# Kernel tuning notes

Hardware: AMD Instinct MI355X
Metric: run time of the kernel (lower is better)

Reference implementation:

```python
import jax, jax.numpy as jnp
import numpy as np

N = 100000      # nodes
E = 3200000     # edges
G = 512         # graphs in batch
H = 64          # hidden_channels
EPS = 1e-5      # BatchNorm eps


def _bn(x, g, b, rm, rv):
    # eval-mode BatchNorm1d using running stats
    return (x - rm) * (g * jax.lax.rsqrt(rv + EPS)) + b


def _gcn(x, W, b, src, dst):
    # PyG GCNConv: add self-loops, sym-normalized scatter-add aggregation
    h = x @ W                                  # [N, H]
    deg = jnp.zeros((N,), x.dtype).at[dst].add(1.0) + 1.0  # +1 self-loop
    dinv = jax.lax.rsqrt(deg)                  # deg^{-1/2}
    coef = (dinv[src] * dinv[dst])[:, None]    # per-edge norm
    agg = jax.ops.segment_sum(h[src] * coef, dst, num_segments=N)
    agg = agg + h * (dinv * dinv)[:, None]     # self-loop message
    return agg + b


def setup_inputs() -> dict:
    key = jax.random.key(0)
    ks = jax.random.split(key, 16)
    d = {}
    d['x'] = jax.random.normal(ks[0], (N, 1), jnp.float32)
    d['src'] = jax.random.randint(ks[1], (E,), 0, N, jnp.int32)
    d['dst'] = jax.random.randint(ks[2], (E,), 0, N, jnp.int32)
    d['batch'] = jnp.sort(jax.random.randint(ks[3], (N,), 0, G, jnp.int32))
    def lin(k, fi, fo):
        s = 1.0 / np.sqrt(fi)
        kw, kb = jax.random.split(k)
        return (jax.random.uniform(kw, (fi, fo), jnp.float32, -s, s),
                jax.random.uniform(kb, (fo,), jnp.float32, -s, s))
    d['w1'], d['b1'] = lin(ks[4], 1, H)
    d['w2'], d['b2'] = lin(ks[5], H, H)
    d['w3'], d['b3'] = lin(ks[6], H, H)
    d['wl1'], d['bl1'] = lin(ks[7], 2 * H, H)
    d['wl2'], d['bl2'] = lin(ks[8], H, 2)
    for i, nm in enumerate(['bn1', 'bn2', 'bn3', 'bnl']):
        kk = jax.random.split(ks[9 + i], 2)
        d[nm + '_g'] = jnp.ones((H,), jnp.float32)
        d[nm + '_b'] = jnp.zeros((H,), jnp.float32)
        d[nm + '_rm'] = 0.1 * jax.random.normal(kk[0], (H,), jnp.float32)
        d[nm + '_rv'] = jnp.abs(1.0 + 0.1 * jax.random.normal(kk[1], (H,), jnp.float32))
    return d


def reference(x, src, dst, batch, w1, b1, w2, b2, w3, b3, wl1, bl1, wl2, bl2,
              bn1_g, bn1_b, bn1_rm, bn1_rv, bn2_g, bn2_b, bn2_rm, bn2_rv,
              bn3_g, bn3_b, bn3_rm, bn3_rv, bnl_g, bnl_b, bnl_rm, bnl_rv):
    # eval mode: dropout is identity, BN uses running stats
    h = jax.nn.relu(_bn(_gcn(x, w1, b1, src, dst), bn1_g, bn1_b, bn1_rm, bn1_rv))
    h = jax.nn.relu(_bn(_gcn(h, w2, b2, src, dst), bn2_g, bn2_b, bn2_rm, bn2_rv))
    h = jax.nn.relu(_bn(_gcn(h, w3, b3, src, dst), bn3_g, bn3_b, bn3_rm, bn3_rv))
    # global mean / max pooling over graphs
    cnt = jax.ops.segment_sum(jnp.ones((N,), h.dtype), batch, num_segments=G)
    x_mean = jax.ops.segment_sum(h, batch, num_segments=G) / jnp.maximum(cnt, 1.0)[:, None]
    x_max = jax.ops.segment_max(h, batch, num_segments=G)
    z = jnp.concatenate([x_mean, x_max], axis=1)          # [G, 2H]
    z = jax.nn.relu(_bn(z @ wl1 + bl1, bnl_g, bnl_b, bnl_rm, bnl_rv))
    return z @ wl2 + bl2                                   # [G, 2]
```

## Files before the change

kernel.cpp:

```cpp
#include <hip/hip_runtime.h>
#include <hip/hip_bf16.h>
#include <cstdio>

#define N_NODES 100000
#define E_EDGES 3200000
#define N_GRAPH 512
#define HDIM 64
#define BN_EPS 1e-5f
#define NBUCKET ((N_NODES + 255) / 256)
#define NCHUNK 256
#define CHUNK ((E_EDGES + NCHUNK - 1) / NCHUNK)
#define SORT_CAP 12288
#define NPW 8
#define WT_STRIDE 68

typedef _Float16 f16;
typedef _Float16 half8 __attribute__((ext_vector_type(8)));


__global__ __launch_bounds__(256) void hist_k(const int* __restrict__ dst,
                                              int* __restrict__ histT) {
    __shared__ int h[NBUCKET];
    int c = blockIdx.x, t = threadIdx.x;
    for (int i = t; i < NBUCKET; i += 256) h[i] = 0;
    __syncthreads();
    int e0 = c * CHUNK;
    int e1 = min(e0 + CHUNK, E_EDGES);
    for (int e = e0 + t; e < e1; e += 256)
        atomicAdd(&h[__builtin_nontemporal_load(dst + e) >> 8], 1);
    __syncthreads();
    for (int i = t; i < NBUCKET; i += 256) histT[i * NCHUNK + c] = h[i];
}

__global__ void scanA_k(const int* __restrict__ histT, int* __restrict__ bucket_base,
                        const float* __restrict__ w1, const float* __restrict__ b1,
                        const float* __restrict__ bg1, const float* __restrict__ bb1,
                        const float* __restrict__ brm1, const float* __restrict__ brv1,
                        float2* __restrict__ m1c1) {
    __shared__ int sh[512];
    int t = threadIdx.x;
    if (t < HDIM) {
        float sc1 = bg1[t] * rsqrtf(brv1[t] + BN_EPS);
        m1c1[t] = make_float2(sc1 * w1[t], (b1[t] - brm1[t]) * sc1 + bb1[t]);
    }
    int sum = 0;
    if (t < NBUCKET) {
        const int* row = histT + t * NCHUNK;
        for (int c = 0; c < NCHUNK; c++) sum += row[c];
    }
    sh[t] = sum;
    __syncthreads();
    for (int off = 1; off < 512; off <<= 1) {
        int add = (t >= off) ? sh[t - off] : 0;
        __syncthreads();
        sh[t] += add;
        __syncthreads();
    }
    if (t < NBUCKET) bucket_base[t] = sh[t] - sum;
    if (t == 0) bucket_base[NBUCKET] = E_EDGES;
}

__global__ __launch_bounds__(NCHUNK) void scanB_k(const int* __restrict__ histT,
                                                  const int* __restrict__ bucket_base,
                                                  int* __restrict__ scannedT) {
    __shared__ int sh[NCHUNK];
    int b = blockIdx.x, t = threadIdx.x;
    int v = histT[b * NCHUNK + t];
    sh[t] = v;
    __syncthreads();
    for (int off = 1; off < NCHUNK; off <<= 1) {
        int add = (t >= off) ? sh[t - off] : 0;
        __syncthreads();
        sh[t] += add;
        __syncthreads();
    }
    scannedT[b * NCHUNK + t] = bucket_base[b] + sh[t] - v;
}

__global__ __launch_bounds__(256) void scatter_k(const int* __restrict__ src,
                                                 const int* __restrict__ dst,
                                                 const int* __restrict__ scannedT,
                                                 int* __restrict__ staging) {
    __shared__ int lcnt[NBUCKET];
    int c = blockIdx.x, t = threadIdx.x;
    for (int i = t; i < NBUCKET; i += 256) lcnt[i] = scannedT[i * NCHUNK + c];
    __syncthreads();
    int e0 = c * CHUNK;
    int e1 = min(e0 + CHUNK, E_EDGES);
    for (int e = e0 + t; e < e1; e += 256) {
        int v = __builtin_nontemporal_load(dst + e);
        int u = __builtin_nontemporal_load(src + e);
        int pos = atomicAdd(&lcnt[v >> 8], 1);
        staging[pos] = u | ((v & 255) << 17);
    }
}


__global__ __launch_bounds__(256) void nodeptr_k(const int* __restrict__ staging,
                                                 const int* __restrict__ bucket_base,
                                                 const float* __restrict__ x,
                                                 int* __restrict__ ptr_raw,
                                                 float* __restrict__ dinv,
                                                 float* __restrict__ xtil,
                                                 int* __restrict__ pbt) {
    __shared__ int hn[256];
    __shared__ int sc[256];
    int t = threadIdx.x, b = blockIdx.x;
    int v0 = b << 8;
    int p0 = bucket_base[b], p1 = bucket_base[b + 1];
    hn[t] = 0;
    __syncthreads();
    int cnt = p1 - p0;
    for (int i = t; i < cnt; i += 256)
        atomicAdd(&hn[staging[p0 + i] >> 17], 1);
    __syncthreads();
    int my = hn[t];
    sc[t] = my;
    __syncthreads();
    for (int off = 1; off < 256; off <<= 1) {
        int add = (t >= off) ? sc[t - off] : 0;
        __syncthreads();
        sc[t] += add;
        __syncthreads();
    }
    int v = v0 + t;
    if (v < N_NODES) {
        ptr_raw[v] = p0 + sc[t] - my;
        float dv = rsqrtf((float)(my + 1));
        dinv[v] = dv;
        xtil[v] = dv * x[v];
    }
    if (b == NBUCKET - 1 && t == 0) ptr_raw[N_NODES] = E_EDGES;
    int pd = (my + 3) & ~3;
    __syncthreads();
    sc[t] = pd;
    __syncthreads();
    for (int off = 1; off < 256; off <<= 1) {
        int add = (t >= off) ? sc[t - off] : 0;
        __syncthreads();
        sc[t] += add;
        __syncthreads();
    }
    if (t == 255) pbt[b] = sc[255];
}

__global__ void scanC_k(const int* __restrict__ pbt, int* __restrict__ pbbase,
                        int* __restrict__ ptr_pad) {
    __shared__ int sh[512];
    int t = threadIdx.x;
    int v = (t < NBUCKET) ? pbt[t] : 0;
    sh[t] = v;
    __syncthreads();
    for (int off = 1; off < 512; off <<= 1) {
        int add = (t >= off) ? sh[t - off] : 0;
        __syncthreads();
        sh[t] += add;
        __syncthreads();
    }
    if (t < NBUCKET) pbbase[t] = sh[t] - v;
    if (t == NBUCKET - 1) {
        pbbase[NBUCKET] = sh[t];
        ptr_pad[N_NODES] = sh[t];
        ptr_pad[N_NODES + 1] = sh[t];
    }
}


__global__ __launch_bounds__(256) void csr_l1_k(const int* __restrict__ staging,
                                                const int* __restrict__ ptr_raw,
                                                const int* __restrict__ bucket_base,
                                                const int* __restrict__ pbbase,
                                                const float* __restrict__ dinv,
                                                const float* __restrict__ xtil,
                                                const float* __restrict__ x,
                                                int* __restrict__ csr,
                                                int* __restrict__ ptr_pad,
                                                float2* __restrict__ pairs) {
    __shared__ int lbase[257];
    __shared__ int plp[257];
    __shared__ int ss[256];
    __shared__ int lcnt[256];
    __shared__ int lds_u[SORT_CAP];
    int t = threadIdx.x, b = blockIdx.x;
    int v0 = b << 8;
    int p0 = bucket_base[b];
    int pb0 = pbbase[b];
    for (int i = t; i < 257; i += 256) {
        int vv = v0 + i;
        lbase[i] = ptr_raw[(vv < N_NODES) ? vv : N_NODES] - p0;
    }
    lcnt[t] = 0;
    __syncthreads();
    int deg = lbase[t + 1] - lbase[t];
    int pd = (deg + 3) & ~3;
    ss[t] = pd;
    __syncthreads();
    for (int off = 1; off < 256; off <<= 1) {
        int add = (t >= off) ? ss[t - off] : 0;
        __syncthreads();
        ss[t] += add;
        __syncthreads();
    }
    plp[t] = ss[t] - pd;
    if (t == 255) plp[256] = ss[255];
    __syncthreads();
    int pcnt = plp[256];
    int cnt = lbase[256];
    int4 sent = {N_NODES, N_NODES, N_NODES, N_NODES};
    int lim4 = min(pcnt, SORT_CAP) >> 2;
    for (int i = t; i < lim4; i += 256) ((int4*)lds_u)[i] = sent;
    __syncthreads();
    for (int i = t; i < cnt; i += 256) {
        int packed = staging[p0 + i];
        int u = packed & 0x1FFFF;
        int vl = packed >> 17;
        int r = atomicAdd(&lcnt[vl], 1);
        int pos = plp[vl] + r;
        if (pos < SORT_CAP) lds_u[pos] = u;
        else csr[pb0 + pos] = u;
    }
    __syncthreads();
    for (int i = t; i < lim4; i += 256)
        ((int4*)(csr + pb0))[i] = ((int4*)lds_u)[i];
    __syncthreads();
    int v = v0 + t;
    if (v < N_NODES) {
        int j0 = plp[t];
        for (int j = j0 + deg; j < j0 + pd; j++)
            if (j >= SORT_CAP) csr[pb0 + j] = N_NODES;
        ptr_pad[v] = pb0 + j0;
        float s = 0.f;
        for (int j = j0; j < j0 + deg; j++) {
            int u = (j < SORT_CAP) ? lds_u[j] : csr[pb0 + j];
            s += xtil[u];
        }
        float dv = dinv[v];
        pairs[v] = make_float2(dv * s + dv * dv * x[v], dv);
    }
    if (b == 0 && t == 0) pairs[N_NODES] = make_float2(0.f, 0.f);
}


__global__ __launch_bounds__(256, 4) void agg_l2_k(
    const float2* __restrict__ pairs, const float2* __restrict__ m1c1,
    f16* __restrict__ xout,
    const int* __restrict__ ptr_pad, const int* __restrict__ csr,
    const float* __restrict__ W2, const float* __restrict__ bias2,
    const float* __restrict__ bg2, const float* __restrict__ bb2,
    const float* __restrict__ brm2, const float* __restrict__ brv2) {
    __shared__ float wsh_t[HDIM * WT_STRIDE];
    __shared__ float sM[HDIM], sC[HDIM];
    __shared__ float a_lds[4][HDIM];
    __shared__ float occ_pad[4096];
    int tid = threadIdx.x;
    occ_pad[tid] = 0.f;
    for (int i = tid; i < HDIM * HDIM; i += 256)
        wsh_t[(i & 63) * WT_STRIDE + (i >> 6)] = W2[i];
    if (tid < HDIM) {
        float sc = bg2[tid] * rsqrtf(brv2[tid] + BN_EPS);
        sM[tid] = sc;
        sC[tid] = (bias2[tid] - brm2[tid]) * sc + bb2[tid];
    }
    __syncthreads();

    int lane = tid & 63;
    int o = lane >> 3, s = lane & 7;
    int f = lane;
    int warp = tid >> 6;
    if (blockIdx.x == 0 && tid < HDIM) xout[(size_t)N_NODES * HDIM + tid] = (f16)0.f;

    float smf = sM[f], scf = sC[f];
    const float4* wt4 = (const float4*)&wsh_t[f * WT_STRIDE];
    const float4* a4 = (const float4*)a_lds[warp];

    float m1[8], c1[8];
#pragma unroll
    for (int i = 0; i < 8; i++) {
        float2 mc = m1c1[s * 8 + i];
        m1[i] = mc.x; c1[i] = mc.y;
    }

    int v0 = (blockIdx.x * 4 + warp) * NPW;
    if (v0 >= N_NODES) return;

    int e = ptr_pad[v0];
    int pe1 = ptr_pad[v0 + 1];
    float2 pv = pairs[v0];
    float2 g0, g1, g2, g3;
    {
        int bb = e + o * 4;
        int4 q = *(const int4*)(csr + bb);
        bool valid = bb < pe1;
        int u0 = valid ? q.x : N_NODES;
        int u1 = valid ? q.y : N_NODES;
        int u2 = valid ? q.z : N_NODES;
        int u3 = valid ? q.w : N_NODES;
        g0 = pairs[u0]; g1 = pairs[u1]; g2 = pairs[u2]; g3 = pairs[u3];
    }

    for (int n = 0; n < NPW; n++) {
        int v = v0 + n;
        int pe2 = ptr_pad[v + 2];
        float acc[8];
        {
            float cf = (o == 0) ? pv.y : 0.f;
#pragma unroll
            for (int i = 0; i < 8; i++)
                acc[i] = cf * fmaxf(m1[i] * pv.x + c1[i], 0.f);
        }
        for (;;) {
            int e2 = e + 32;
            bool last = (e2 >= pe1);
            int nb = last ? pe1 : e2;
            int nbound = last ? ((n + 1 < NPW) ? pe2 : pe1) : pe1;
            int bb2 = nb + o * 4;
            int4 q = *(const int4*)(csr + bb2);
            {
                float2 p = g0;
#pragma unroll
                for (int i = 0; i < 8; i++) acc[i] += p.y * fmaxf(m1[i] * p.x + c1[i], 0.f);
                p = g1;
#pragma unroll
                for (int i = 0; i < 8; i++) acc[i] += p.y * fmaxf(m1[i] * p.x + c1[i], 0.f);
                p = g2;
#pragma unroll
                for (int i = 0; i < 8; i++) acc[i] += p.y * fmaxf(m1[i] * p.x + c1[i], 0.f);
                p = g3;
#pragma unroll
                for (int i = 0; i < 8; i++) acc[i] += p.y * fmaxf(m1[i] * p.x + c1[i], 0.f);
            }
            bool valid = bb2 < nbound;
            int u0 = valid ? q.x : N_NODES;
            int u1 = valid ? q.y : N_NODES;
            int u2 = valid ? q.z : N_NODES;
            int u3 = valid ? q.w : N_NODES;
            g0 = pairs[u0]; g1 = pairs[u1]; g2 = pairs[u2]; g3 = pairs[u3];
            if (last) break;
            e = e2;
        }
        e = pe1;
        float2 pv_n = pairs[v + 1];
#pragma unroll
        for (int i = 0; i < 8; i++) {
            acc[i] += __shfl_xor(acc[i], 8);
            acc[i] += __shfl_xor(acc[i], 16);
            acc[i] += __shfl_xor(acc[i], 32);
        }
        if (o == 0) {
            float4* d4 = (float4*)&a_lds[warp][s * 8];
            d4[0] = make_float4(acc[0], acc[1], acc[2], acc[3]);
            d4[1] = make_float4(acc[4], acc[5], acc[6], acc[7]);
        }
        asm volatile("s_waitcnt lgkmcnt(0)" ::: "memory");
        float ovp0 = 0.f, ovp1 = 0.f, ovp2 = 0.f, ovp3 = 0.f;
#pragma unroll
        for (int k4 = 0; k4 < 16; k4++) {
            float4 w4 = wt4[k4];
            float4 av = a4[k4];
            ovp0 += av.x * w4.x;
            ovp1 += av.y * w4.y;
            ovp2 += av.z * w4.z;
            ovp3 += av.w * w4.w;
        }
        float ov = (ovp0 + ovp1) + (ovp2 + ovp3);
        float val = fmaxf(pv.y * ov * smf + scf, 0.f);
        xout[(size_t)v * HDIM + f] = (f16)(pv.y * val);
        pe1 = pe2;
        pv = pv_n;
    }
}


__global__ __launch_bounds__(256, 4) void agg_gemm_k(
    const f16* __restrict__ xin, f16* __restrict__ xout,
    const int* __restrict__ ptr_pad, const int* __restrict__ csr,
    const float2* __restrict__ pairs,
    const float* __restrict__ W, const float* __restrict__ bias,
    const float* __restrict__ bg, const float* __restrict__ bb,
    const float* __restrict__ brm, const float* __restrict__ brv) {
    __shared__ float wsh_t[HDIM * WT_STRIDE];
    __shared__ float sM[HDIM], sC[HDIM];
    __shared__ float a_lds[4][HDIM];
    __shared__ float occ_pad[4096];
    int tid = threadIdx.x;
    occ_pad[tid] = 0.f;
    for (int i = tid; i < HDIM * HDIM; i += 256)
        wsh_t[(i & 63) * WT_STRIDE + (i >> 6)] = W[i];
    if (tid < HDIM) {
        float sc = bg[tid] * rsqrtf(brv[tid] + BN_EPS);
        sM[tid] = sc;
        sC[tid] = (bias[tid] - brm[tid]) * sc + bb[tid];
    }
    __syncthreads();

    int lane = tid & 63;
    int o = lane >> 3, s = lane & 7;
    int f = lane;
    int warp = tid >> 6;
    const half8* __restrict__ xin8 = (const half8*)xin;

    float smf = sM[f], scf = sC[f];
    const float4* wt4 = (const float4*)&wsh_t[f * WT_STRIDE];
    const float4* a4 = (const float4*)a_lds[warp];

    int v0 = (blockIdx.x * 4 + warp) * NPW;
    if (v0 >= N_NODES) return;

    int e = ptr_pad[v0];
    int pe1 = ptr_pad[v0 + 1];
    half8 rs = xin8[(size_t)v0 * 8 + s];
    float dv = pairs[v0].y;
    half8 g0, g1, g2, g3;
    {
        int bb = e + o * 4;
        int4 q = *(const int4*)(csr + bb);
        bool valid = bb < pe1;
        int u0 = valid ? q.x : N_NODES;
        int u1 = valid ? q.y : N_NODES;
        int u2 = valid ? q.z : N_NODES;
        int u3 = valid ? q.w : N_NODES;
        g0 = xin8[(size_t)u0 * 8 + s];
        g1 = xin8[(size_t)u1 * 8 + s];
        g2 = xin8[(size_t)u2 * 8 + s];
        g3 = xin8[(size_t)u3 * 8 + s];
    }

    for (int n = 0; n < NPW; n++) {
        int v = v0 + n;
        int pe2 = ptr_pad[v + 2];
        float acc[8];
        {
            float cf = (o == 0) ? 1.f : 0.f;
#pragma unroll
            for (int i = 0; i < 8; i++) acc[i] = cf * (float)rs[i];
        }
        for (;;) {
            int e2 = e + 32;
            bool last = (e2 >= pe1);
            int nb = last ? pe1 : e2;
            int nbound = last ? ((n + 1 < NPW) ? pe2 : pe1) : pe1;
            int bb2 = nb + o * 4;
            int4 q = *(const int4*)(csr + bb2);
            {
#pragma unroll
                for (int i = 0; i < 8; i++) acc[i] += (float)g0[i];
#pragma unroll
                for (int i = 0; i < 8; i++) acc[i] += (float)g1[i];
#pragma unroll
                for (int i = 0; i < 8; i++) acc[i] += (float)g2[i];
#pragma unroll
                for (int i = 0; i < 8; i++) acc[i] += (float)g3[i];
            }
            bool valid = bb2 < nbound;
            int u0 = valid ? q.x : N_NODES;
            int u1 = valid ? q.y : N_NODES;
            int u2 = valid ? q.z : N_NODES;
            int u3 = valid ? q.w : N_NODES;
            g0 = xin8[(size_t)u0 * 8 + s];
            g1 = xin8[(size_t)u1 * 8 + s];
            g2 = xin8[(size_t)u2 * 8 + s];
            g3 = xin8[(size_t)u3 * 8 + s];
            if (last) break;
            e = e2;
        }
        e = pe1;
        half8 rs_n = xin8[(size_t)(v + 1) * 8 + s];
        float dv_n = pairs[v + 1].y;
#pragma unroll
        for (int i = 0; i < 8; i++) {
            acc[i] += __shfl_xor(acc[i], 8);
            acc[i] += __shfl_xor(acc[i], 16);
            acc[i] += __shfl_xor(acc[i], 32);
        }
        if (o == 0) {
            float4* d4 = (float4*)&a_lds[warp][s * 8];
            d4[0] = make_float4(acc[0], acc[1], acc[2], acc[3]);
            d4[1] = make_float4(acc[4], acc[5], acc[6], acc[7]);
        }
        asm volatile("s_waitcnt lgkmcnt(0)" ::: "memory");
        float ovp0 = 0.f, ovp1 = 0.f, ovp2 = 0.f, ovp3 = 0.f;
#pragma unroll
        for (int k4 = 0; k4 < 16; k4++) {
            float4 w4 = wt4[k4];
            float4 av = a4[k4];
            ovp0 += av.x * w4.x;
            ovp1 += av.y * w4.y;
            ovp2 += av.z * w4.z;
            ovp3 += av.w * w4.w;
        }
        float ov = (ovp0 + ovp1) + (ovp2 + ovp3);
        float val = fmaxf(dv * ov * smf + scf, 0.f);
        xout[(size_t)v * HDIM + f] = (f16)val;
        pe1 = pe2;
        rs = rs_n;
        dv = dv_n;
    }
}


__device__ inline int lower_bound_i(const int* __restrict__ a, int n, int val) {
    int lo = 0, hi = n;
    while (lo < hi) {
        int mid = (lo + hi) >> 1;
        if (a[mid] < val) lo = mid + 1; else hi = mid;
    }
    return lo;
}

__global__ void pool_mlp_k(const f16* __restrict__ x, const int* __restrict__ batch,
                           const float* __restrict__ wl1, const float* __restrict__ bl1,
                           const float* __restrict__ wl2, const float* __restrict__ bl2,
                           const float* __restrict__ bg, const float* __restrict__ bb,
                           const float* __restrict__ brm, const float* __restrict__ brv,
                           float* __restrict__ out) {
    int g = blockIdx.x;
    int tid = threadIdx.x;
    int w = tid >> 6;
    int f = tid & 63;
    int start = lower_bound_i(batch, N_NODES, g);
    int end = lower_bound_i(batch, N_NODES, g + 1);
    float sum = 0.f;
    float mx = -3.402823466e38f;
#pragma unroll 2
    for (int v = start + w; v < end; v += 4) {
        float val = (float)x[(size_t)v * HDIM + f];
        sum += val;
        mx = fmaxf(mx, val);
    }
    __shared__ float ssum[4][HDIM], smax[4][HDIM];
    __shared__ float zs[2 * HDIM];
    ssum[w][f] = sum;
    smax[w][f] = mx;
    __syncthreads();
    if (tid < 64) {
        float sm = ssum[0][f] + ssum[1][f] + ssum[2][f] + ssum[3][f];
        float m = fmaxf(fmaxf(smax[0][f], smax[1][f]), fmaxf(smax[2][f], smax[3][f]));
        float cnt = (float)(end - start);
        zs[f] = sm / fmaxf(cnt, 1.f);
        zs[HDIM + f] = m;
    }
    __syncthreads();
    if (tid >= 64) return;

    float o = bl1[f];
#pragma unroll 8
    for (int k = 0; k < 2 * HDIM; k++) {
        o += zs[k] * wl1[k * HDIM + f];
    }
    float sc = bg[f] * rsqrtf(brv[f] + BN_EPS);
    o = fmaxf((o - brm[f]) * sc + bb[f], 0.f);

    float p0 = o * wl2[f * 2 + 0];
    float p1 = o * wl2[f * 2 + 1];
    for (int off = 32; off > 0; off >>= 1) {
        p0 += __shfl_down(p0, off);
        p1 += __shfl_down(p1, off);
    }
    if (f == 0) {
        out[g * 2 + 0] = p0 + bl2[0];
        out[g * 2 + 1] = p1 + bl2[1];
    }
}


extern "C" void kernel_launch(void* const* d_in, const int* in_sizes, int n_in,
                              void* d_out, int out_size, void* d_ws, size_t ws_size,
                              hipStream_t stream) {
    const float* x    = (const float*)d_in[0];
    const int* src    = (const int*)d_in[1];
    const int* dst    = (const int*)d_in[2];
    const int* batch  = (const int*)d_in[3];
    const float* w1   = (const float*)d_in[4];
    const float* b1   = (const float*)d_in[5];
    const float* w2   = (const float*)d_in[6];
    const float* b2   = (const float*)d_in[7];
    const float* w3   = (const float*)d_in[8];
    const float* b3   = (const float*)d_in[9];
    const float* wl1  = (const float*)d_in[10];
    const float* bl1  = (const float*)d_in[11];
    const float* wl2  = (const float*)d_in[12];
    const float* bl2  = (const float*)d_in[13];
    const float* bn1g = (const float*)d_in[14];
    const float* bn1b = (const float*)d_in[15];
    const float* bn1rm = (const float*)d_in[16];
    const float* bn1rv = (const float*)d_in[17];
    const float* bn2g = (const float*)d_in[18];
    const float* bn2b = (const float*)d_in[19];
    const float* bn2rm = (const float*)d_in[20];
    const float* bn2rv = (const float*)d_in[21];
    const float* bn3g = (const float*)d_in[22];
    const float* bn3b = (const float*)d_in[23];
    const float* bn3rm = (const float*)d_in[24];
    const float* bn3rv = (const float*)d_in[25];
    const float* bnlg = (const float*)d_in[26];
    const float* bnlb = (const float*)d_in[27];
    const float* bnlrm = (const float*)d_in[28];
    const float* bnlrv = (const float*)d_in[29];
    float* out = (float*)d_out;

    char* ws = (char*)d_ws;
    size_t off = 0;
    auto alloc = [&](size_t bytes) -> char* {
        off = (off + 255) & ~(size_t)255;
        char* p = ws + off;
        off += bytes;
        return p;
    };
    int*    histT    = (int*)alloc((size_t)NBUCKET * NCHUNK * 4);
    int*    scannedT = (int*)alloc((size_t)NBUCKET * NCHUNK * 4);
    int*    bbase    = (int*)alloc((NBUCKET + 1) * 4);
    int*    pbt      = (int*)alloc(NBUCKET * 4);
    int*    pbbase   = (int*)alloc((NBUCKET + 1) * 4);
    int*    staging  = (int*)alloc((size_t)E_EDGES * 4);
    int*    csr      = (int*)alloc(((size_t)E_EDGES + 4 * N_NODES + 64) * 4);
    int*    ptr_raw  = (int*)alloc(((size_t)N_NODES + 1) * 4);
    int*    ptr_pad  = (int*)alloc(((size_t)N_NODES + 2) * 4);
    float*  dinv     = (float*)alloc((size_t)N_NODES * 4);
    float*  xtil     = (float*)alloc((size_t)N_NODES * 4);
    float2* pairs    = (float2*)alloc(((size_t)N_NODES + 1) * 8);
    float2* m1c1     = (float2*)alloc((size_t)HDIM * 8);
    f16*    x2       = (f16*)alloc(((size_t)N_NODES + 1) * HDIM * 2);
    f16*    x3       = (f16*)alloc((size_t)N_NODES * HDIM * 2);
    if (off > ws_size) {
        fprintf(stderr, "kernel_launch: ws too small (%zu > %zu)\n", off, ws_size);
    }

    const int NB_AGG = (N_NODES + 4 * NPW - 1) / (4 * NPW);

    hist_k<<<NCHUNK, 256, 0, stream>>>(dst, histT);
    scanA_k<<<1, 512, 0, stream>>>(histT, bbase, w1, b1, bn1g, bn1b, bn1rm, bn1rv, m1c1);
    scanB_k<<<NBUCKET, NCHUNK, 0, stream>>>(histT, bbase, scannedT);
    scatter_k<<<NCHUNK, 256, 0, stream>>>(src, dst, scannedT, staging);
    nodeptr_k<<<NBUCKET, 256, 0, stream>>>(staging, bbase, x, ptr_raw, dinv, xtil, pbt);
    scanC_k<<<1, 512, 0, stream>>>(pbt, pbbase, ptr_pad);
    csr_l1_k<<<NBUCKET, 256, 0, stream>>>(staging, ptr_raw, bbase, pbbase,
                                          dinv, xtil, x, csr, ptr_pad, pairs);

    agg_l2_k<<<NB_AGG, 256, 0, stream>>>(pairs, m1c1, x2, ptr_pad, csr,
                                         w2, b2, bn2g, bn2b, bn2rm, bn2rv);
    agg_gemm_k<<<NB_AGG, 256, 0, stream>>>(x2, x3, ptr_pad, csr, pairs,
                                           w3, b3, bn3g, bn3b, bn3rm, bn3rv);

    pool_mlp_k<<<N_GRAPH, 256, 0, stream>>>(x3, batch, wl1, bl1, wl2, bl2,
                                            bnlg, bnlb, bnlrm, bnlrv, out);
}
```

Before: 413.7 us.

## Restructure CSR build: fixed padded bucket offsets, separate layer-1 aggregation kernel

Bucket totals are now accumulated atomically in the histogram kernel, so the scan no longer sums the full histogram rows. The nodeptr and scanC kernels are removed: each bucket's padded CSR base becomes its raw offset rounded up plus a fixed per-bucket slack (PADSTRIDE), and the unused slack is filled with sentinels, which drops one pass over staging and a serial scan. Layer-1 aggregation moves out of the per-bucket CSR kernel into a new kernel that reduces each node's neighbours across half-waves, replacing one-thread-per-node serial loops. The occupancy padding LDS arrays in the later aggregation kernels are also removed. The costs are an extra memset and launch, and a larger CSR buffer; correctness relies on the padded degree sum of each bucket fitting within its slack.

```diff
diff --git a/kernel.cpp b/kernel.cpp
--- a/kernel.cpp
+++ b/kernel.cpp
@@ -12,14 +12,17 @@
 #define CHUNK ((E_EDGES + NCHUNK - 1) / NCHUNK)
 #define SORT_CAP 12288
 #define NPW 8
+#define NPL 8
 #define WT_STRIDE 68
+#define PADSTRIDE 772
 
 typedef _Float16 f16;
 typedef _Float16 half8 __attribute__((ext_vector_type(8)));
 
 
 __global__ __launch_bounds__(256) void hist_k(const int* __restrict__ dst,
-                                              int* __restrict__ histT) {
+                                              int* __restrict__ histT,
+                                              int* __restrict__ btot) {
     __shared__ int h[NBUCKET];
     int c = blockIdx.x, t = threadIdx.x;
     for (int i = t; i < NBUCKET; i += 256) h[i] = 0;
@@ -29,10 +32,14 @@
     for (int e = e0 + t; e < e1; e += 256)
         atomicAdd(&h[__builtin_nontemporal_load(dst + e) >> 8], 1);
     __syncthreads();
-    for (int i = t; i < NBUCKET; i += 256) histT[i * NCHUNK + c] = h[i];
-}
-
-__global__ void scanA_k(const int* __restrict__ histT, int* __restrict__ bucket_base,
+    for (int i = t; i < NBUCKET; i += 256) {
+        int hv = h[i];
+        histT[i * NCHUNK + c] = hv;
+        atomicAdd(&btot[i], hv);
+    }
+}
+
+__global__ void scanA_k(const int* __restrict__ btot, int* __restrict__ bucket_base,
                         const float* __restrict__ w1, const float* __restrict__ b1,
                         const float* __restrict__ bg1, const float* __restrict__ bb1,
                         const float* __restrict__ brm1, const float* __restrict__ brv1,
@@ -43,11 +50,7 @@
         float sc1 = bg1[t] * rsqrtf(brv1[t] + BN_EPS);
         m1c1[t] = make_float2(sc1 * w1[t], (b1[t] - brm1[t]) * sc1 + bb1[t]);
     }
-    int sum = 0;
-    if (t < NBUCKET) {
-        const int* row = histT + t * NCHUNK;
-        for (int c = 0; c < NCHUNK; c++) sum += row[c];
-    }
+    int sum = (t < NBUCKET) ? btot[t] : 0;
     sh[t] = sum;
     __syncthreads();
     for (int off = 1; off < 512; off <<= 1) {
@@ -96,102 +99,32 @@
 }
 
 
-__global__ __launch_bounds__(256) void nodeptr_k(const int* __restrict__ staging,
-                                                 const int* __restrict__ bucket_base,
-                                                 const float* __restrict__ x,
-                                                 int* __restrict__ ptr_raw,
-                                                 float* __restrict__ dinv,
-                                                 float* __restrict__ xtil,
-                                                 int* __restrict__ pbt) {
-    __shared__ int hn[256];
-    __shared__ int sc[256];
-    int t = threadIdx.x, b = blockIdx.x;
-    int v0 = b << 8;
-    int p0 = bucket_base[b], p1 = bucket_base[b + 1];
-    hn[t] = 0;
-    __syncthreads();
-    int cnt = p1 - p0;
-    for (int i = t; i < cnt; i += 256)
-        atomicAdd(&hn[staging[p0 + i] >> 17], 1);
-    __syncthreads();
-    int my = hn[t];
-    sc[t] = my;
-    __syncthreads();
-    for (int off = 1; off < 256; off <<= 1) {
-        int add = (t >= off) ? sc[t - off] : 0;
-        __syncthreads();
-        sc[t] += add;
-        __syncthreads();
-    }
-    int v = v0 + t;
-    if (v < N_NODES) {
-        ptr_raw[v] = p0 + sc[t] - my;
-        float dv = rsqrtf((float)(my + 1));
-        dinv[v] = dv;
-        xtil[v] = dv * x[v];
-    }
-    if (b == NBUCKET - 1 && t == 0) ptr_raw[N_NODES] = E_EDGES;
-    int pd = (my + 3) & ~3;
-    __syncthreads();
-    sc[t] = pd;
-    __syncthreads();
-    for (int off = 1; off < 256; off <<= 1) {
-        int add = (t >= off) ? sc[t - off] : 0;
-        __syncthreads();
-        sc[t] += add;
-        __syncthreads();
-    }
-    if (t == 255) pbt[b] = sc[255];
-}
-
-__global__ void scanC_k(const int* __restrict__ pbt, int* __restrict__ pbbase,
-                        int* __restrict__ ptr_pad) {
-    __shared__ int sh[512];
-    int t = threadIdx.x;
-    int v = (t < NBUCKET) ? pbt[t] : 0;
-    sh[t] = v;
-    __syncthreads();
-    for (int off = 1; off < 512; off <<= 1) {
-        int add = (t >= off) ? sh[t - off] : 0;
-        __syncthreads();
-        sh[t] += add;
-        __syncthreads();
-    }
-    if (t < NBUCKET) pbbase[t] = sh[t] - v;
-    if (t == NBUCKET - 1) {
-        pbbase[NBUCKET] = sh[t];
-        ptr_pad[N_NODES] = sh[t];
-        ptr_pad[N_NODES + 1] = sh[t];
-    }
-}
-
-
-__global__ __launch_bounds__(256) void csr_l1_k(const int* __restrict__ staging,
-                                                const int* __restrict__ ptr_raw,
+__global__ __launch_bounds__(256) void bucket_k(const int* __restrict__ staging,
                                                 const int* __restrict__ bucket_base,
-                                                const int* __restrict__ pbbase,
-                                                const float* __restrict__ dinv,
-                                                const float* __restrict__ xtil,
                                                 const float* __restrict__ x,
                                                 int* __restrict__ csr,
                                                 int* __restrict__ ptr_pad,
-                                                float2* __restrict__ pairs) {
-    __shared__ int lbase[257];
+                                                float* __restrict__ dinv,
+                                                float* __restrict__ xtil) {
+    __shared__ int hn[256];
     __shared__ int plp[257];
     __shared__ int ss[256];
     __shared__ int lcnt[256];
     __shared__ int lds_u[SORT_CAP];
     int t = threadIdx.x, b = blockIdx.x;
     int v0 = b << 8;
-    int p0 = bucket_base[b];
-    int pb0 = pbbase[b];
-    for (int i = t; i < 257; i += 256) {
-        int vv = v0 + i;
-        lbase[i] = ptr_raw[(vv < N_NODES) ? vv : N_NODES] - p0;
-    }
+    int p0 = bucket_base[b], p1 = bucket_base[b + 1];
+    int p0a = (p0 + 3) & ~3;
+    int pb0 = p0a + PADSTRIDE * b;
+    int gcap = ((p1 + 3) & ~3) + PADSTRIDE * (b + 1) - pb0;
+    hn[t] = 0;
     lcnt[t] = 0;
     __syncthreads();
-    int deg = lbase[t + 1] - lbase[t];
+    int cnt = p1 - p0;
+    for (int i = t; i < cnt; i += 256)
+        atomicAdd(&hn[staging[p0 + i] >> 17], 1);
+    __syncthreads();
+    int deg = hn[t];
     int pd = (deg + 3) & ~3;
     ss[t] = pd;
     __syncthreads();
@@ -205,10 +138,23 @@
     if (t == 255) plp[256] = ss[255];
     __syncthreads();
     int pcnt = plp[256];
-    int cnt = lbase[256];
+    int v = v0 + t;
+    if (v < N_NODES) {
+        float dv = rsqrtf((float)(deg + 1));
+        dinv[v] = dv;
+        xtil[v] = dv * x[v];
+        ptr_pad[v] = pb0 + plp[t];
+    }
+    if (b == NBUCKET - 1 && t == 0) {
+        ptr_pad[N_NODES] = pb0 + pcnt;
+        ptr_pad[N_NODES + 1] = pb0 + pcnt;
+    }
+    if (b == 0 && t == 0) xtil[N_NODES] = 0.f;
     int4 sent = {N_NODES, N_NODES, N_NODES, N_NODES};
     int lim4 = min(pcnt, SORT_CAP) >> 2;
     for (int i = t; i < lim4; i += 256) ((int4*)lds_u)[i] = sent;
+    int4* gout = (int4*)(csr + pb0);
+    for (int i = (pcnt >> 2) + t; i < (gcap >> 2); i += 256) gout[i] = sent;
     __syncthreads();
     for (int i = t; i < cnt; i += 256) {
         int packed = staging[p0 + i];
@@ -221,23 +167,44 @@
     }
     __syncthreads();
     for (int i = t; i < lim4; i += 256)
-        ((int4*)(csr + pb0))[i] = ((int4*)lds_u)[i];
-    __syncthreads();
-    int v = v0 + t;
+        gout[i] = ((int4*)lds_u)[i];
     if (v < N_NODES) {
         int j0 = plp[t];
         for (int j = j0 + deg; j < j0 + pd; j++)
             if (j >= SORT_CAP) csr[pb0 + j] = N_NODES;
-        ptr_pad[v] = pb0 + j0;
+    }
+}
+
+
+__global__ __launch_bounds__(256, 8) void agg_l1_k(const int* __restrict__ ptr_pad,
+                                                   const int* __restrict__ csr,
+                                                   const float* __restrict__ dinv,
+                                                   const float* __restrict__ xtil,
+                                                   const float* __restrict__ x,
+                                                   float2* __restrict__ pairs) {
+    int tid = threadIdx.x;
+    int wave = tid >> 6, lane = tid & 63;
+    int h = lane >> 5, l = lane & 31;
+    if (blockIdx.x == 0 && tid == 0) pairs[N_NODES] = make_float2(0.f, 0.f);
+    int v0 = (blockIdx.x * 4 + wave) * NPL;
+    if (v0 >= N_NODES) return;
+    for (int n = 0; n < NPL; n += 2) {
+        int v = v0 + n + h;
         float s = 0.f;
-        for (int j = j0; j < j0 + deg; j++) {
-            int u = (j < SORT_CAP) ? lds_u[j] : csr[pb0 + j];
-            s += xtil[u];
-        }
-        float dv = dinv[v];
-        pairs[v] = make_float2(dv * s + dv * dv * x[v], dv);
-    }
-    if (b == 0 && t == 0) pairs[N_NODES] = make_float2(0.f, 0.f);
+        int e0 = 0, e1 = 0;
+        if (v < N_NODES) { e0 = ptr_pad[v]; e1 = ptr_pad[v + 1]; }
+        for (int e = e0 + l; e < e1; e += 32)
+            s += xtil[csr[e]];
+        s += __shfl_xor(s, 1);
+        s += __shfl_xor(s, 2);
+        s += __shfl_xor(s, 4);
+        s += __shfl_xor(s, 8);
+        s += __shfl_xor(s, 16);
+        if (v < N_NODES && l == 0) {
+            float dv = dinv[v];
+            pairs[v] = make_float2(dv * s + dv * dv * x[v], dv);
+        }
+    }
 }
 
 
@@ -251,9 +218,7 @@
     __shared__ float wsh_t[HDIM * WT_STRIDE];
     __shared__ float sM[HDIM], sC[HDIM];
     __shared__ float a_lds[4][HDIM];
-    __shared__ float occ_pad[4096];
     int tid = threadIdx.x;
-    occ_pad[tid] = 0.f;
     for (int i = tid; i < HDIM * HDIM; i += 256)
         wsh_t[(i & 63) * WT_STRIDE + (i >> 6)] = W2[i];
     if (tid < HDIM) {
@@ -381,9 +346,7 @@
     __shared__ float wsh_t[HDIM * WT_STRIDE];
     __shared__ float sM[HDIM], sC[HDIM];
     __shared__ float a_lds[4][HDIM];
-    __shared__ float occ_pad[4096];
     int tid = threadIdx.x;
-    occ_pad[tid] = 0.f;
     for (int i = tid; i < HDIM * HDIM; i += 256)
         wsh_t[(i & 63) * WT_STRIDE + (i >> 6)] = W[i];
     if (tid < HDIM) {
@@ -609,14 +572,12 @@
     int*    histT    = (int*)alloc((size_t)NBUCKET * NCHUNK * 4);
     int*    scannedT = (int*)alloc((size_t)NBUCKET * NCHUNK * 4);
     int*    bbase    = (int*)alloc((NBUCKET + 1) * 4);
-    int*    pbt      = (int*)alloc(NBUCKET * 4);
-    int*    pbbase   = (int*)alloc((NBUCKET + 1) * 4);
+    int*    btot     = (int*)alloc(NBUCKET * 4);
     int*    staging  = (int*)alloc((size_t)E_EDGES * 4);
-    int*    csr      = (int*)alloc(((size_t)E_EDGES + 4 * N_NODES + 64) * 4);
-    int*    ptr_raw  = (int*)alloc(((size_t)N_NODES + 1) * 4);
+    int*    csr      = (int*)alloc(((size_t)E_EDGES + (size_t)PADSTRIDE * NBUCKET + 512) * 4);
     int*    ptr_pad  = (int*)alloc(((size_t)N_NODES + 2) * 4);
     float*  dinv     = (float*)alloc((size_t)N_NODES * 4);
-    float*  xtil     = (float*)alloc((size_t)N_NODES * 4);
+    float*  xtil     = (float*)alloc(((size_t)N_NODES + 1) * 4);
     float2* pairs    = (float2*)alloc(((size_t)N_NODES + 1) * 8);
     float2* m1c1     = (float2*)alloc((size_t)HDIM * 8);
     f16*    x2       = (f16*)alloc(((size_t)N_NODES + 1) * HDIM * 2);
@@ -627,14 +588,13 @@
 
     const int NB_AGG = (N_NODES + 4 * NPW - 1) / (4 * NPW);
 
-    hist_k<<<NCHUNK, 256, 0, stream>>>(dst, histT);
-    scanA_k<<<1, 512, 0, stream>>>(histT, bbase, w1, b1, bn1g, bn1b, bn1rm, bn1rv, m1c1);
+    hipMemsetAsync(btot, 0, (size_t)NBUCKET * 4, stream);
+    hist_k<<<NCHUNK, 256, 0, stream>>>(dst, histT, btot);
+    scanA_k<<<1, 512, 0, stream>>>(btot, bbase, w1, b1, bn1g, bn1b, bn1rm, bn1rv, m1c1);
     scanB_k<<<NBUCKET, NCHUNK, 0, stream>>>(histT, bbase, scannedT);
     scatter_k<<<NCHUNK, 256, 0, stream>>>(src, dst, scannedT, staging);
-    nodeptr_k<<<NBUCKET, 256, 0, stream>>>(staging, bbase, x, ptr_raw, dinv, xtil, pbt);
-    scanC_k<<<1, 512, 0, stream>>>(pbt, pbbase, ptr_pad);
-    csr_l1_k<<<NBUCKET, 256, 0, stream>>>(staging, ptr_raw, bbase, pbbase,
-                                          dinv, xtil, x, csr, ptr_pad, pairs);
+    bucket_k<<<NBUCKET, 256, 0, stream>>>(staging, bbase, x, csr, ptr_pad, dinv, xtil);
+    agg_l1_k<<<NB_AGG, 256, 0, stream>>>(ptr_pad, csr, dinv, xtil, x, pairs);
 
     agg_l2_k<<<NB_AGG, 256, 0, stream>>>(pairs, m1c1, x2, ptr_pad, csr,
                                          w2, b2, bn2g, bn2b, bn2rm, bn2rv);
```

Result: no change. 420.8 us (+1.7%).
